# Optimization experiments

Measured on AMD Instinct MI355X. Metric: run time of the kernel, lower is better.

## Reference

```python
import jax, jax.numpy as jnp
import numpy as np

D_MODEL = 1024
N_HEADS = 16
D_KEYS = 64
D_LLM = 4096
B, L, S = 8, 1024, 1000
HD = N_HEADS * D_KEYS  # 1024


def setup_inputs() -> dict:
    key = jax.random.key(0)
    ks = jax.random.split(key, 12)
    sd = lambda fan_in: 1.0 / np.sqrt(fan_in)
    return {
        "target_embedding": jax.random.normal(ks[0], (B, L, D_MODEL), jnp.float32),
        "source_embedding": jax.random.normal(ks[1], (S, D_LLM), jnp.float32),
        "value_embedding": jax.random.normal(ks[2], (S, D_LLM), jnp.float32),
        "Wq": jax.random.normal(ks[3], (D_MODEL, HD), jnp.float32) * sd(D_MODEL),
        "bq": jnp.zeros((HD,), jnp.float32),
        "Wk": jax.random.normal(ks[4], (D_LLM, HD), jnp.float32) * sd(D_LLM),
        "bk": jnp.zeros((HD,), jnp.float32),
        "Wv": jax.random.normal(ks[5], (D_LLM, HD), jnp.float32) * sd(D_LLM),
        "bv": jnp.zeros((HD,), jnp.float32),
        "Wo": jax.random.normal(ks[6], (HD, D_LLM), jnp.float32) * sd(HD),
        "bo": jnp.zeros((D_LLM,), jnp.float32),
        "alpha": jnp.asarray(1.0, jnp.float32),
        "beta": jnp.asarray(0.5, jnp.float32),
    }


def reference(target_embedding, source_embedding, value_embedding,
              Wq, bq, Wk, bk, Wv, bv, Wo, bo, alpha, beta):
    # Projections
    q = (target_embedding @ Wq + bq).reshape(B, L, N_HEADS, D_KEYS)   # blhe
    k = (source_embedding @ Wk + bk).reshape(S, N_HEADS, D_KEYS)      # she
    v = (value_embedding @ Wv + bv).reshape(S, N_HEADS, D_KEYS)       # she
    # Reprogramming attention with alpha/beta scaling
    scale = 1.0 / np.sqrt(D_KEYS)
    scores = jnp.einsum('blhe,she->bhls', alpha * q, beta * k)        # BxHxLxS
    A = jax.nn.softmax(scale * scores, axis=-1)  # dropout is identity in eval
    out = jnp.einsum('bhls,she->blhe', A, v)
    out = out.reshape(B, L, HD)
    return out @ Wo + bo                                              # B,L,d_llm
```

## Files before the change

kernel.cpp:

```cpp
#include <hip/hip_runtime.h>

typedef unsigned short u16;
typedef __attribute__((ext_vector_type(8))) short short8;
typedef __attribute__((ext_vector_type(4))) float floatx4;

#define LOG2E 1.4426950408889634f

__device__ __forceinline__ u16 f2bf(float f) {
    unsigned u = __builtin_bit_cast(unsigned, f);
    u += 0x7fffu + ((u >> 16) & 1u);
    return (u16)(u >> 16);
}

__device__ __forceinline__ void gl2lds16(const void* g, void* l) {
    __builtin_amdgcn_global_load_lds((const __attribute__((address_space(1))) void*)g,
                                     (__attribute__((address_space(3))) void*)l,
                                     16, 0, 0);
}

__global__ __launch_bounds__(256) void conv_all(const float* __restrict__ T, u16* __restrict__ Tb,
                                                const float* __restrict__ Se, u16* __restrict__ Seb,
                                                const float* __restrict__ Ve, u16* __restrict__ Veb) {
    int g = blockIdx.x * 256 + threadIdx.x;
    const float* s; u16* d; int i; int nsrc;
    if (g < 2097152)      { s = T;  d = Tb;  i = g * 4;               nsrc = 8388608; }
    else if (g < 3145728) { s = Se; d = Seb; i = (g - 2097152) * 4;   nsrc = 4096000; }
    else                  { s = Ve; d = Veb; i = (g - 3145728) * 4;   nsrc = 4096000; }
    ushort4 o;
    if (i < nsrc) {
        float4 v = *(const float4*)(s + i);
        o.x = f2bf(v.x); o.y = f2bf(v.y); o.z = f2bf(v.z); o.w = f2bf(v.w);
    } else {
        o = make_ushort4(0, 0, 0, 0);
    }
    *(ushort4*)(d + i) = o;
}

__device__ __forceinline__ void transpose_core(const float* __restrict__ W, u16* __restrict__ Wt,
                                               int Kd, int Nd, int kx, int ny) {
    __shared__ u16 t[64][65];
    const int tid = threadIdx.x;
    const int k0 = kx * 64, n0 = ny * 64;
#pragma unroll
    for (int i = 0; i < 16; i++) {
        int r = i * 4 + (tid >> 6), c = tid & 63;
        t[r][c] = f2bf(W[(size_t)(k0 + r) * Nd + n0 + c]);
    }
    __syncthreads();
#pragma unroll
    for (int i = 0; i < 16; i++) {
        int n = i * 4 + (tid >> 6), k = tid & 63;
        Wt[(size_t)(n0 + n) * Kd + k0 + k] = t[k][n];
    }
}

__global__ __launch_bounds__(256) void transpose3(const float* __restrict__ Wq, u16* __restrict__ WqT,
                                                  const float* __restrict__ Wk, u16* __restrict__ WkT,
                                                  const float* __restrict__ Wv, u16* __restrict__ WvT) {
    int id = blockIdx.x;
    if (id < 256)       transpose_core(Wq, WqT, 1024, 1024, id & 15, id >> 4);
    else if (id < 1280) { int t = id - 256;  transpose_core(Wk, WkT, 4096, 1024, t & 63, t >> 6); }
    else                { int t = id - 1280; transpose_core(Wv, WvT, 4096, 1024, t & 63, t >> 6); }
}

__global__ __launch_bounds__(256) void transpose_wo(const float* __restrict__ Wo, u16* __restrict__ WoT) {
    int id = blockIdx.x;
    transpose_core(Wo, WoT, 1024, 4096, id & 15, id >> 4);
}

__device__ __forceinline__
void gemm_core(const u16* __restrict__ A, const u16* __restrict__ Bt,
               const float* __restrict__ bias, void* __restrict__ Cout,
               int M, int N, int K, int mode, float mult, int m0, int n0,
               u16* sA, u16* sB) {
    const int tid = threadIdx.x;
    const int wave = tid >> 6, lane = tid & 63;
    const int quad = lane >> 4, l16 = lane & 15;
    const int wm = (wave >> 1) * 64, wn = (wave & 1) * 64;

    floatx4 acc[4][4];
#pragma unroll
    for (int i = 0; i < 4; i++)
#pragma unroll
        for (int j = 0; j < 4; j++) acc[i][j] = (floatx4){0.f, 0.f, 0.f, 0.f};

    const u16* Ag = A + (size_t)m0 * K;
    const u16* Bg = Bt + (size_t)n0 * K;
    const int sr = tid >> 3, sc = (tid & 7) * 8;

    for (int k0 = 0; k0 < K; k0 += 64) {
#pragma unroll
        for (int i = 0; i < 4; i++) {
            int r = i * 32 + sr;
            gl2lds16(Ag + (size_t)r * K + k0 + sc, sA + i * 2048 + wave * 512);
            gl2lds16(Bg + (size_t)r * K + k0 + sc, sB + i * 2048 + wave * 512);
        }
        __syncthreads();
#pragma unroll
        for (int kk = 0; kk < 64; kk += 32) {
            short8 af[4], bf[4];
#pragma unroll
            for (int i = 0; i < 4; i++)
                af[i] = *(const short8*)&sA[(wm + i * 16 + l16) * 64 + kk + quad * 8];
#pragma unroll
            for (int j = 0; j < 4; j++)
                bf[j] = *(const short8*)&sB[(wn + j * 16 + l16) * 64 + kk + quad * 8];
#pragma unroll
            for (int i = 0; i < 4; i++)
#pragma unroll
                for (int j = 0; j < 4; j++)
                    acc[i][j] = __builtin_amdgcn_mfma_f32_16x16x32_bf16(af[i], bf[j], acc[i][j], 0, 0, 0);
        }
        __syncthreads();
    }

#pragma unroll
    for (int i = 0; i < 4; i++) {
#pragma unroll
        for (int j = 0; j < 4; j++) {
            int col = n0 + wn + j * 16 + l16;
            float bv = bias[col];
#pragma unroll
            for (int r = 0; r < 4; r++) {
                int row = m0 + wm + i * 16 + quad * 4 + r;
                float v = (acc[i][j][r] + bv) * mult;
                if (mode == 3) {
                    ((float*)Cout)[(size_t)row * N + col] = v;
                } else if (mode == 2) {
                    ((u16*)Cout)[(size_t)col * M + row] = f2bf(v);
                } else {
                    ((u16*)Cout)[(size_t)row * N + col] = f2bf(v);
                }
            }
        }
    }
}

__global__ __launch_bounds__(256, 2)
void gemm_qkv(const u16* __restrict__ Tb, const u16* __restrict__ WqT, const float* __restrict__ bq,
              const u16* __restrict__ Seb, const u16* __restrict__ WkT, const float* __restrict__ bk,
              const u16* __restrict__ Veb, const u16* __restrict__ WvT, const float* __restrict__ bv,
              u16* __restrict__ Qb, u16* __restrict__ Kb, u16* __restrict__ VTb,
              const float* __restrict__ alphaP, const float* __restrict__ betaP) {
    __shared__ u16 sA[128 * 64];
    __shared__ u16 sB[128 * 64];
    int yy = blockIdx.y, n0 = blockIdx.x * 128;
    if (yy < 64) {
        float mult = alphaP[0] * betaP[0] * 0.125f * LOG2E;
        gemm_core(Tb, WqT, bq, Qb, 8192, 1024, 1024, 1, mult, yy * 128, n0, sA, sB);
    } else if (yy < 72) {
        gemm_core(Seb, WkT, bk, Kb, 1024, 1024, 4096, 0, 1.0f, (yy - 64) * 128, n0, sA, sB);
    } else {
        gemm_core(Veb, WvT, bv, VTb, 1024, 1024, 4096, 2, 1.0f, (yy - 72) * 128, n0, sA, sB);
    }
}

__global__ __launch_bounds__(256, 2)
void gemm_final(const u16* __restrict__ A, const u16* __restrict__ Bt,
                const float* __restrict__ bias, float* __restrict__ Cout) {
    __shared__ u16 sA[128 * 64];
    __shared__ u16 sB[128 * 64];
    gemm_core(A, Bt, bias, Cout, 8192, 4096, 1024, 3, 1.0f, blockIdx.y * 128, blockIdx.x * 128, sA, sB);
}

__global__ __launch_bounds__(256, 2)
void attn_kernel(const u16* __restrict__ Q, const u16* __restrict__ Kb,
                 const u16* __restrict__ VT, u16* __restrict__ O) {
    __shared__ u16 sK[128 * 64];
    __shared__ u16 sV[64 * 128];
    __shared__ u16 sP[128 * 128];
    const int tid = threadIdx.x;
    const int wave = tid >> 6, lane = tid & 63;
    const int quad = lane >> 4, l16 = lane & 15;
    const int l7 = l16 & 7;
    const int bid = blockIdx.x;
    const int qt = bid & 7, h = (bid >> 3) & 15, b = bid >> 7;

    const u16* Qbase = Q + ((size_t)(b * 1024 + qt * 128 + wave * 32)) * 1024 + h * 64;
    short8 qf[2][2];
#pragma unroll
    for (int i = 0; i < 2; i++)
#pragma unroll
        for (int kk = 0; kk < 2; kk++)
            qf[i][kk] = *(const short8*)&Qbase[(size_t)(i * 16 + l16) * 1024 + kk * 32 + quad * 8];

    float psum[2] = {0.f, 0.f};
    floatx4 oacc[2][4];
#pragma unroll
    for (int i = 0; i < 2; i++)
#pragma unroll
        for (int n = 0; n < 4; n++) oacc[i][n] = (floatx4){0.f, 0.f, 0.f, 0.f};

    for (int st = 0; st < 8; ++st) {
#pragma unroll
        for (int i = 0; i < 4; i++) {
            int r = i * 32 + wave * 8 + (lane >> 3);
            int c = ((lane & 7) ^ ((lane >> 3) & 7)) * 8;
            gl2lds16(Kb + (size_t)(st * 128 + r) * 1024 + h * 64 + c, sK + i * 2048 + wave * 512);
        }
#pragma unroll
        for (int i = 0; i < 4; i++) {
            int r = i * 16 + wave * 4 + (lane >> 4);
            int c = ((lane & 15) ^ ((wave * 4 + (lane >> 4)) & 7)) * 8;
            gl2lds16(VT + (size_t)(h * 64 + r) * 1024 + st * 128 + c, sV + i * 2048 + wave * 512);
        }
        __syncthreads();

        floatx4 sacc[2][8];
#pragma unroll
        for (int i = 0; i < 2; i++)
#pragma unroll
            for (int j = 0; j < 8; j++) sacc[i][j] = (floatx4){0.f, 0.f, 0.f, 0.f};
#pragma unroll
        for (int kk = 0; kk < 2; kk++) {
            short8 kf[8];
#pragma unroll
            for (int j = 0; j < 8; j++)
                kf[j] = *(const short8*)&sK[(j * 16 + l16) * 64 + (((kk * 4 + quad) ^ l7) * 8)];
#pragma unroll
            for (int i = 0; i < 2; i++)
#pragma unroll
                for (int j = 0; j < 8; j++)
                    sacc[i][j] = __builtin_amdgcn_mfma_f32_16x16x32_bf16(kf[j], qf[i][kk], sacc[i][j], 0, 0, 0);
        }

#pragma unroll
        for (int i = 0; i < 2; i++) {
            const int rowbase = (wave * 32 + i * 16 + l16) * 128;
#pragma unroll
            for (int j = 0; j < 8; j++) {
                float p0 = exp2f(sacc[i][j][0]);
                float p1 = exp2f(sacc[i][j][1]);
                float p2 = exp2f(sacc[i][j][2]);
                float p3 = exp2f(sacc[i][j][3]);
                if (st == 7) {
                    if (j == 7 || (j == 6 && quad >= 2)) { p0 = p1 = p2 = p3 = 0.f; }
                }
                psum[i] += (p0 + p1) + (p2 + p3);
                uint2 val;
                val.x = (unsigned)f2bf(p0) | ((unsigned)f2bf(p1) << 16);
                val.y = (unsigned)f2bf(p2) | ((unsigned)f2bf(p3) << 16);
                int chunk = (2 * j + (quad >> 1)) ^ l7;
                *(uint2*)&sP[rowbase + chunk * 8 + (quad & 1) * 4] = val;
            }
        }

#pragma unroll
        for (int c = 0; c < 4; c++) {
            short8 pf[2], vf[4];
#pragma unroll
            for (int i = 0; i < 2; i++)
                pf[i] = *(const short8*)&sP[(wave * 32 + i * 16 + l16) * 128 + (((c * 4 + quad) ^ l7) * 8)];
#pragma unroll
            for (int n = 0; n < 4; n++)
                vf[n] = *(const short8*)&sV[(n * 16 + l16) * 128 + (((c * 4 + quad) ^ l7) * 8)];
#pragma unroll
            for (int i = 0; i < 2; i++)
#pragma unroll
                for (int n = 0; n < 4; n++)
                    oacc[i][n] = __builtin_amdgcn_mfma_f32_16x16x32_bf16(pf[i], vf[n], oacc[i][n], 0, 0, 0);
        }
        __syncthreads();
    }

#pragma unroll
    for (int i = 0; i < 2; i++) {
        psum[i] += __shfl_xor(psum[i], 16);
        psum[i] += __shfl_xor(psum[i], 32);
    }

    u16* Obase = O + ((size_t)(b * 1024 + qt * 128 + wave * 32)) * 1024 + h * 64;
#pragma unroll
    for (int i = 0; i < 2; i++) {
#pragma unroll
        for (int r = 0; r < 4; r++) {
            float l = __shfl(psum[i], (lane & 48) | (quad * 4 + r));
            float linv = 1.0f / l;
#pragma unroll
            for (int n = 0; n < 4; n++)
                Obase[(size_t)(i * 16 + quad * 4 + r) * 1024 + n * 16 + l16] = f2bf(oacc[i][n][r] * linv);
        }
    }
}

extern "C" void kernel_launch(void* const* d_in, const int* in_sizes, int n_in,
                              void* d_out, int out_size, void* d_ws, size_t ws_size,
                              hipStream_t stream) {
    const float* T     = (const float*)d_in[0];
    const float* Se    = (const float*)d_in[1];
    const float* Ve    = (const float*)d_in[2];
    const float* Wq    = (const float*)d_in[3];
    const float* bq    = (const float*)d_in[4];
    const float* Wk    = (const float*)d_in[5];
    const float* bk    = (const float*)d_in[6];
    const float* Wv    = (const float*)d_in[7];
    const float* bv    = (const float*)d_in[8];
    const float* Wo    = (const float*)d_in[9];
    const float* bo    = (const float*)d_in[10];
    const float* alpha = (const float*)d_in[11];
    const float* beta  = (const float*)d_in[12];

    char* ws = (char*)d_ws;
    size_t off = 0;
    auto alloc = [&](size_t bytes) { size_t o = off; off += (bytes + 255) & ~(size_t)255; return o; };

    u16* Tb  = (u16*)(ws + alloc((size_t)8192 * 1024 * 2));
    u16* Seb = (u16*)(ws + alloc((size_t)1024 * 4096 * 2));
    u16* Veb = (u16*)(ws + alloc((size_t)1024 * 4096 * 2));
    u16* WqT = (u16*)(ws + alloc((size_t)1024 * 1024 * 2));
    u16* WkT = (u16*)(ws + alloc((size_t)1024 * 4096 * 2));
    u16* WvT = (u16*)(ws + alloc((size_t)1024 * 4096 * 2));
    u16* Qb  = (u16*)(ws + alloc((size_t)8192 * 1024 * 2));
    u16* Kb  = (u16*)(ws + alloc((size_t)1024 * 1024 * 2));
    u16* VTb = (u16*)(ws + alloc((size_t)1024 * 1024 * 2));
    u16* Ob  = Tb;
    u16* WoT = Veb;

    conv_all<<<16384, 256, 0, stream>>>(T, Tb, Se, Seb, Ve, Veb);
    transpose3<<<2304, 256, 0, stream>>>(Wq, WqT, Wk, WkT, Wv, WvT);
    gemm_qkv<<<dim3(8, 80), 256, 0, stream>>>(Tb, WqT, bq, Seb, WkT, bk, Veb, WvT, bv,
                                              Qb, Kb, VTb, alpha, beta);
    transpose_wo<<<1024, 256, 0, stream>>>(Wo, WoT);
    attn_kernel<<<1024, 256, 0, stream>>>(Qb, Kb, VTb, Ob);
    gemm_final<<<dim3(32, 64), 256, 0, stream>>>(Ob, WoT, bo, (float*)d_out);
}
```

Baseline: 471.3 us.

## Split-K the K/V projections with a reduction kernel and swizzle GEMM block order

The K and V projections (K=4096) are split into four K-chunks that write fp32 partials, so 512 blocks instead of 128 handle that long-K work alongside the Q blocks. A new reduce kernel sums the partials, adds bias, converts to bf16, and also absorbs the Wo transpose. Block indices in gemm_qkv and gemm_final are remapped so neighbouring blocks share tiles, aiming for better L2 reuse across XCDs. The cost is extra fp32 partial traffic (32MB written and read) plus one more pass.

After: 442.4 us. 6.1% less time.

```diff
diff --git a/kernel.cpp b/kernel.cpp
--- a/kernel.cpp
+++ b/kernel.cpp
@@ -63,15 +63,11 @@
     else                { int t = id - 1280; transpose_core(Wv, WvT, 4096, 1024, t & 63, t >> 6); }
 }
 
-__global__ __launch_bounds__(256) void transpose_wo(const float* __restrict__ Wo, u16* __restrict__ WoT) {
-    int id = blockIdx.x;
-    transpose_core(Wo, WoT, 1024, 4096, id & 15, id >> 4);
-}
-
 __device__ __forceinline__
 void gemm_core(const u16* __restrict__ A, const u16* __restrict__ Bt,
                const float* __restrict__ bias, void* __restrict__ Cout,
-               int M, int N, int K, int mode, float mult, int m0, int n0,
+               int M, int N, int Kstride, int Klen, int koff,
+               int mode, float mult, int m0, int n0,
                u16* sA, u16* sB) {
     const int tid = threadIdx.x;
     const int wave = tid >> 6, lane = tid & 63;
@@ -84,16 +80,16 @@
 #pragma unroll
         for (int j = 0; j < 4; j++) acc[i][j] = (floatx4){0.f, 0.f, 0.f, 0.f};
 
-    const u16* Ag = A + (size_t)m0 * K;
-    const u16* Bg = Bt + (size_t)n0 * K;
+    const u16* Ag = A + (size_t)m0 * Kstride + koff;
+    const u16* Bg = Bt + (size_t)n0 * Kstride + koff;
     const int sr = tid >> 3, sc = (tid & 7) * 8;
 
-    for (int k0 = 0; k0 < K; k0 += 64) {
+    for (int k0 = 0; k0 < Klen; k0 += 64) {
 #pragma unroll
         for (int i = 0; i < 4; i++) {
             int r = i * 32 + sr;
-            gl2lds16(Ag + (size_t)r * K + k0 + sc, sA + i * 2048 + wave * 512);
-            gl2lds16(Bg + (size_t)r * K + k0 + sc, sB + i * 2048 + wave * 512);
+            gl2lds16(Ag + (size_t)r * Kstride + k0 + sc, sA + i * 2048 + wave * 512);
+            gl2lds16(Bg + (size_t)r * Kstride + k0 + sc, sB + i * 2048 + wave * 512);
         }
         __syncthreads();
 #pragma unroll
@@ -119,13 +115,15 @@
 #pragma unroll
         for (int j = 0; j < 4; j++) {
             int col = n0 + wn + j * 16 + l16;
-            float bv = bias[col];
+            float bv = (mode >= 4) ? 0.0f : bias[col];
 #pragma unroll
             for (int r = 0; r < 4; r++) {
                 int row = m0 + wm + i * 16 + quad * 4 + r;
                 float v = (acc[i][j][r] + bv) * mult;
-                if (mode == 3) {
+                if (mode == 3 || mode == 4) {
                     ((float*)Cout)[(size_t)row * N + col] = v;
+                } else if (mode == 5) {
+                    ((float*)Cout)[(size_t)col * M + row] = v;
                 } else if (mode == 2) {
                     ((u16*)Cout)[(size_t)col * M + row] = f2bf(v);
                 } else {
@@ -138,20 +136,71 @@
 
 __global__ __launch_bounds__(256, 2)
 void gemm_qkv(const u16* __restrict__ Tb, const u16* __restrict__ WqT, const float* __restrict__ bq,
-              const u16* __restrict__ Seb, const u16* __restrict__ WkT, const float* __restrict__ bk,
-              const u16* __restrict__ Veb, const u16* __restrict__ WvT, const float* __restrict__ bv,
-              u16* __restrict__ Qb, u16* __restrict__ Kb, u16* __restrict__ VTb,
+              const u16* __restrict__ Seb, const u16* __restrict__ WkT,
+              const u16* __restrict__ Veb, const u16* __restrict__ WvT,
+              u16* __restrict__ Qb, float* __restrict__ KP, float* __restrict__ VPT,
               const float* __restrict__ alphaP, const float* __restrict__ betaP) {
     __shared__ u16 sA[128 * 64];
     __shared__ u16 sB[128 * 64];
-    int yy = blockIdx.y, n0 = blockIdx.x * 128;
-    if (yy < 64) {
+    int b0 = blockIdx.x;
+    int bid = (b0 & 7) * 128 + (b0 >> 3);
+    if (bid < 512) {
+        int m = bid >> 3, n = bid & 7;
         float mult = alphaP[0] * betaP[0] * 0.125f * LOG2E;
-        gemm_core(Tb, WqT, bq, Qb, 8192, 1024, 1024, 1, mult, yy * 128, n0, sA, sB);
-    } else if (yy < 72) {
-        gemm_core(Seb, WkT, bk, Kb, 1024, 1024, 4096, 0, 1.0f, (yy - 64) * 128, n0, sA, sB);
+        gemm_core(Tb, WqT, bq, Qb, 8192, 1024, 1024, 1024, 0,
+                  1, mult, m * 128, n * 128, sA, sB);
+    } else if (bid < 768) {
+        int t = bid - 512;
+        int kc = t >> 6, m = (t >> 3) & 7, n = t & 7;
+        gemm_core(Seb, WkT, nullptr, KP + (size_t)kc * 1048576, 1024, 1024, 4096, 1024, kc * 1024,
+                  4, 1.0f, m * 128, n * 128, sA, sB);
     } else {
-        gemm_core(Veb, WvT, bv, VTb, 1024, 1024, 4096, 2, 1.0f, (yy - 72) * 128, n0, sA, sB);
+        int t = bid - 768;
+        int kc = t >> 6, m = (t >> 3) & 7, n = t & 7;
+        gemm_core(Veb, WvT, nullptr, VPT + (size_t)kc * 1048576, 1024, 1024, 4096, 1024, kc * 1024,
+                  5, 1.0f, m * 128, n * 128, sA, sB);
+    }
+}
+
+__global__ __launch_bounds__(256)
+void reduce_wo(const float* __restrict__ KP, const float* __restrict__ bk, u16* __restrict__ Kb,
+               const float* __restrict__ VPT, const float* __restrict__ bv, u16* __restrict__ VTb,
+               const float* __restrict__ Wo, u16* __restrict__ WoT) {
+    int id = blockIdx.x;
+    if (id >= 2048) {
+        int t = id - 2048;
+        transpose_core(Wo, WoT, 1024, 4096, t & 15, t >> 4);
+        return;
+    }
+    const int tid = threadIdx.x;
+    if (id < 1024) {
+        int r = id, c = tid * 4;
+        size_t base = (size_t)r * 1024 + c;
+        float4 a0 = *(const float4*)(KP + base);
+        float4 a1 = *(const float4*)(KP + 1048576 + base);
+        float4 a2 = *(const float4*)(KP + 2097152 + base);
+        float4 a3 = *(const float4*)(KP + 3145728 + base);
+        float4 bb = *(const float4*)(bk + c);
+        ushort4 o;
+        o.x = f2bf(a0.x + a1.x + a2.x + a3.x + bb.x);
+        o.y = f2bf(a0.y + a1.y + a2.y + a3.y + bb.y);
+        o.z = f2bf(a0.z + a1.z + a2.z + a3.z + bb.z);
+        o.w = f2bf(a0.w + a1.w + a2.w + a3.w + bb.w);
+        *(ushort4*)(Kb + base) = o;
+    } else {
+        int d = id - 1024, s = tid * 4;
+        size_t base = (size_t)d * 1024 + s;
+        float4 a0 = *(const float4*)(VPT + base);
+        float4 a1 = *(const float4*)(VPT + 1048576 + base);
+        float4 a2 = *(const float4*)(VPT + 2097152 + base);
+        float4 a3 = *(const float4*)(VPT + 3145728 + base);
+        float bvv = bv[d];
+        ushort4 o;
+        o.x = f2bf(a0.x + a1.x + a2.x + a3.x + bvv);
+        o.y = f2bf(a0.y + a1.y + a2.y + a3.y + bvv);
+        o.z = f2bf(a0.z + a1.z + a2.z + a3.z + bvv);
+        o.w = f2bf(a0.w + a1.w + a2.w + a3.w + bvv);
+        *(ushort4*)(VTb + base) = o;
     }
 }
 
@@ -160,7 +209,10 @@
                 const float* __restrict__ bias, float* __restrict__ Cout) {
     __shared__ u16 sA[128 * 64];
     __shared__ u16 sB[128 * 64];
-    gemm_core(A, Bt, bias, Cout, 8192, 4096, 1024, 3, 1.0f, blockIdx.y * 128, blockIdx.x * 128, sA, sB);
+    int b0 = blockIdx.x;
+    int bid = (b0 & 7) * 256 + (b0 >> 3);
+    int m = bid >> 5, n = bid & 31;
+    gemm_core(A, Bt, bias, Cout, 8192, 4096, 1024, 1024, 0, 3, 1.0f, m * 128, n * 128, sA, sB);
 }
 
 __global__ __launch_bounds__(256, 2)
@@ -313,14 +365,16 @@
     u16* Qb  = (u16*)(ws + alloc((size_t)8192 * 1024 * 2));
     u16* Kb  = (u16*)(ws + alloc((size_t)1024 * 1024 * 2));
     u16* VTb = (u16*)(ws + alloc((size_t)1024 * 1024 * 2));
+    float* KP  = (float*)(ws + alloc((size_t)4 * 1024 * 1024 * 4));
+    float* VPT = (float*)(ws + alloc((size_t)4 * 1024 * 1024 * 4));
     u16* Ob  = Tb;
     u16* WoT = Veb;
 
     conv_all<<<16384, 256, 0, stream>>>(T, Tb, Se, Seb, Ve, Veb);
     transpose3<<<2304, 256, 0, stream>>>(Wq, WqT, Wk, WkT, Wv, WvT);
-    gemm_qkv<<<dim3(8, 80), 256, 0, stream>>>(Tb, WqT, bq, Seb, WkT, bk, Veb, WvT, bv,
-                                              Qb, Kb, VTb, alpha, beta);
-    transpose_wo<<<1024, 256, 0, stream>>>(Wo, WoT);
+    gemm_qkv<<<1024, 256, 0, stream>>>(Tb, WqT, bq, Seb, WkT, Veb, WvT,
+                                       Qb, KP, VPT, alpha, beta);
+    reduce_wo<<<3072, 256, 0, stream>>>(KP, bk, Kb, VPT, bv, VTb, Wo, WoT);
     attn_kernel<<<1024, 256, 0, stream>>>(Qb, Kb, VTb, Ob);
-    gemm_final<<<dim3(32, 64), 256, 0, stream>>>(Ob, WoT, bo, (float*)d_out);
-}
+    gemm_final<<<2048, 256, 0, stream>>>(Ob, WoT, bo, (float*)d_out);
+}
```
